# Kernel tuning notes

Hardware: AMD Instinct MI355X
Metric: run time of the kernel (lower is better)

The kernel has to match this reference:

```python
import jax, jax.numpy as jnp
import numpy as np

TOP_K = 2          # n_activated_experts
ROUTE_SCALE = 1.0  # args.route_scale


def setup_inputs() -> dict:
    key = jax.random.key(0)
    ks = jax.random.split(key, 12)
    B, S, D, I, E = 8, 2048, 512, 1024, 8
    SH = 2 * I  # n_shared_experts * moe_inter_dim
    std = 0.02
    return {
        "x": jax.random.normal(ks[0], (B, S, D), jnp.float32),
        "gate_w": (jax.random.normal(ks[1], (E, D), jnp.float32) * std),
        "w1": (jax.random.normal(ks[2], (E, D, I), jnp.float32) * std),
        "w2": (jax.random.normal(ks[3], (E, I, D), jnp.float32) * std),
        "w3": (jax.random.normal(ks[4], (E, D, I), jnp.float32) * std),
        "sw1": (jax.random.normal(ks[5], (D, SH), jnp.float32) * std),
        "sb1": jnp.zeros((SH,), jnp.float32),
        "sw2": (jax.random.normal(ks[6], (SH, D), jnp.float32) * std),
        "sb2": jnp.zeros((D,), jnp.float32),
        "sw3": (jax.random.normal(ks[7], (D, SH), jnp.float32) * std),
        "sb3": jnp.zeros((SH,), jnp.float32),
    }


def reference(x, gate_w, w1, w2, w3, sw1, sb1, sw2, sb2, sw3, sb3):
    B, S, D = x.shape
    xt = x.reshape(-1, D)              # [T, D] tokens
    T = xt.shape[0]
    E = gate_w.shape[0]

    # --- Gate: sigmoid scores, top-k, renormalized weights ---
    scores = jax.nn.sigmoid(xt @ gate_w.T)                 # [T, E]
    topv, topi = jax.lax.top_k(scores, TOP_K)              # [T, K]
    wts = topv / jnp.sum(topv, axis=-1, keepdims=True)
    wts = wts * ROUTE_SCALE

    # Dense combine weights: zero for non-selected experts -> faithful to
    # the torch masked scatter-accumulate over the expert loop.
    cw = jnp.zeros((T, E), xt.dtype).at[jnp.arange(T)[:, None], topi].add(wts)

    # --- Routed SwiGLU experts (ffn_bias=False) ---
    y = jnp.zeros_like(xt)
    for e in range(E):  # fixed small structural loop over experts
        h = jax.nn.silu(xt @ w1[e]) * (xt @ w3[e])         # [T, I]
        y = y + cw[:, e:e + 1] * (h @ w2[e])               # combine

    # --- Load-balance aux loss L_ExpBal ---
    counts = jnp.zeros((E,), xt.dtype).at[topi.reshape(-1)].add(1.0)
    f_i = E * counts / (TOP_K * T)
    P_i = cw.sum(axis=0) / T   # per-expert sum of routed weights
    L_ExpBal = jnp.sum(f_i * P_i)

    # --- Shared experts MLP (biased Linear, SwiGLU) ---
    z = (jax.nn.silu(xt @ sw1 + sb1) * (xt @ sw3 + sb3)) @ sw2 + sb2

    return (y + z).reshape(B, S, D), L_ExpBal
```

## Files before the change

kernel.cpp:

```cpp
#include <hip/hip_runtime.h>
#include <math.h>
#include <stdint.h>

#define T_TOK 16384
#define DDIM  512
#define IDIM  1024
#define NEXP  8
#define SHDIM 2048
#define MPAD  34816
#define GBLK  256

typedef unsigned short u16;
typedef short bf16x8 __attribute__((ext_vector_type(8)));
typedef float f32x4 __attribute__((ext_vector_type(4)));

__device__ __forceinline__ u16 f2bf(float f) {
    unsigned u = __float_as_uint(f);
    u += 0x7FFF + ((u >> 16) & 1);
    return (u16)(u >> 16);
}
__device__ __forceinline__ float bf2f(u16 h) {
    return __uint_as_float((unsigned)h << 16);
}

__device__ __forceinline__ void gload_lds16(const void* g, void* l) {
    __builtin_amdgcn_global_load_lds(
        (const __attribute__((address_space(1))) void*)g,
        (__attribute__((address_space(3))) void*)l, 16, 0, 0);
}

__device__ __forceinline__ int ksw(int r) { return (r & 3) ^ ((r >> 2) & 3); }

__global__ void k_zero(int* cursors) {
    int i = threadIdx.x;
    if (i < NEXP) cursors[i] = 0;
}

__global__ __launch_bounds__(256) void k_gate(
    const float* __restrict__ x, const float* __restrict__ gw,
    int* __restrict__ topi, float* __restrict__ wts,
    int* __restrict__ pcnt, float* __restrict__ pps, u16* __restrict__ xb)
{
    __shared__ int   cnt[NEXP];
    __shared__ float ps[NEXP];
    const int tid = threadIdx.x;
    if (tid < NEXP) { cnt[tid] = 0; ps[tid] = 0.f; }
    __syncthreads();
    const int wid = tid >> 6, lane = tid & 63;

    const float4* gw4 = (const float4*)gw;
    float4 g0[NEXP], g1[NEXP];
#pragma unroll
    for (int e = 0; e < NEXP; e++) {
        g0[e] = gw4[e * 128 + lane];
        g1[e] = gw4[e * 128 + 64 + lane];
    }

    const int t0 = blockIdx.x * 64 + wid * 16;
    for (int u = 0; u < 16; u++) {
        int t = t0 + u;
        const float4* xr4 = (const float4*)(x + (size_t)t * DDIM);
        float4 v0 = xr4[lane];
        float4 v1 = xr4[64 + lane];
        ushort4 o0 = { f2bf(v0.x), f2bf(v0.y), f2bf(v0.z), f2bf(v0.w) };
        ushort4 o1 = { f2bf(v1.x), f2bf(v1.y), f2bf(v1.z), f2bf(v1.w) };
        ushort4* xbo = (ushort4*)(xb + (size_t)t * DDIM);
        xbo[lane] = o0;
        xbo[64 + lane] = o1;
        float acc[NEXP];
#pragma unroll
        for (int e = 0; e < NEXP; e++) {
            acc[e] = v0.x * g0[e].x + v0.y * g0[e].y + v0.z * g0[e].z + v0.w * g0[e].w
                   + v1.x * g1[e].x + v1.y * g1[e].y + v1.z * g1[e].z + v1.w * g1[e].w;
        }
#pragma unroll
        for (int e = 0; e < NEXP; e++) {
#pragma unroll
            for (int off = 32; off; off >>= 1) acc[e] += __shfl_xor(acc[e], off, 64);
        }
        if (lane == 0) {
            float s[NEXP];
#pragma unroll
            for (int e = 0; e < NEXP; e++) s[e] = 1.f / (1.f + expf(-acc[e]));
            int i1 = 0; float v1s = s[0];
#pragma unroll
            for (int e = 1; e < NEXP; e++) if (s[e] > v1s) { v1s = s[e]; i1 = e; }
            int i2 = -1; float v2s = -1.f;
#pragma unroll
            for (int e = 0; e < NEXP; e++) if (e != i1 && s[e] > v2s) { v2s = s[e]; i2 = e; }
            float inv = 1.f / (v1s + v2s);
            float wa = v1s * inv, wb = v2s * inv;
            topi[2 * t] = i1; topi[2 * t + 1] = i2;
            wts[2 * t] = wa;  wts[2 * t + 1] = wb;
            atomicAdd(&cnt[i1], 1); atomicAdd(&cnt[i2], 1);
            atomicAdd(&ps[i1], wa); atomicAdd(&ps[i2], wb);
        }
    }
    __syncthreads();
    if (tid < NEXP) {
        pcnt[blockIdx.x * NEXP + tid] = cnt[tid];
        pps[blockIdx.x * NEXP + tid]  = ps[tid];
    }
}

__global__ void k_scan(const int* __restrict__ pcnt, const float* __restrict__ pps,
                       int* __restrict__ off_pad, float* __restrict__ out_loss)
{
    __shared__ int   scnt[8][NEXP];
    __shared__ float sps[8][NEXP];
    int tid = threadIdx.x;
    if (tid < 64) {
        int e = tid & 7, part = tid >> 3;
        int c = 0; float p = 0.f;
        for (int b = part * 32; b < part * 32 + 32; b++) {
            c += pcnt[b * NEXP + e];
            p += pps[b * NEXP + e];
        }
        scnt[part][e] = c; sps[part][e] = p;
    }
    __syncthreads();
    if (tid == 0) {
        int off = 0; float L = 0.f;
        for (int e = 0; e < NEXP; e++) {
            int c = 0; float p = 0.f;
            for (int q = 0; q < 8; q++) { c += scnt[q][e]; p += sps[q][e]; }
            off_pad[e] = off;
            off += (c + 255) & ~255;
            float f = (float)NEXP * (float)c / (float)(2 * T_TOK);
            L += f * (p / (float)T_TOK);
        }
        off_pad[NEXP] = off;
        out_loss[0] = L;
    }
}

__global__ void k_fillperm(int* __restrict__ perm, u16* __restrict__ zpad) {
    int i = blockIdx.x * blockDim.x + threadIdx.x;
    if (i < MPAD) perm[i] = -1;
    if (blockIdx.x == 0 && threadIdx.x < 256) ((unsigned*)zpad)[threadIdx.x] = 0u;
}

__global__ __launch_bounds__(256) void k_scatter(
    const int* __restrict__ topi, const float* __restrict__ wts,
    const int* __restrict__ off_pad, int* __restrict__ cursors,
    int* __restrict__ perm, float* __restrict__ pw, int* __restrict__ inv)
{
    __shared__ int lcnt[NEXP];
    __shared__ int lbase[NEXP];
    int tid = threadIdx.x;
    if (tid < NEXP) lcnt[tid] = 0;
    __syncthreads();
    int t = blockIdx.x * 256 + tid;
    int e0 = topi[2 * t], e1 = topi[2 * t + 1];
    int p0 = atomicAdd(&lcnt[e0], 1);
    int p1 = atomicAdd(&lcnt[e1], 1);
    __syncthreads();
    if (tid < NEXP) lbase[tid] = atomicAdd(&cursors[tid], lcnt[tid]);
    __syncthreads();
    int s0 = off_pad[e0] + lbase[e0] + p0;
    int s1 = off_pad[e1] + lbase[e1] + p1;
    perm[s0] = t; pw[s0] = wts[2 * t];
    perm[s1] = t; pw[s1] = wts[2 * t + 1];
    inv[2 * t] = s0; inv[2 * t + 1] = s1;
}

__global__ __launch_bounds__(256) void k_transpose(const float* __restrict__ src,
                                                   u16* __restrict__ dst, int R, int C,
                                                   int rmul, int radd, int zrows)
{
    __shared__ u16 t[64][68];
    const float* s = src + (size_t)blockIdx.z * R * C;
    u16* d = dst + (size_t)blockIdx.z * zrows * R;
    int r0 = blockIdx.y * 64, c0 = blockIdx.x * 64;
    int tid = threadIdx.x;
    int lr = tid >> 4, lc = (tid & 15) * 4;
#pragma unroll
    for (int u = 0; u < 4; u++) {
        int r = lr + u * 16;
        float4 v = *(const float4*)&s[(size_t)(r0 + r) * C + c0 + lc];
        t[lc + 0][r] = f2bf(v.x);
        t[lc + 1][r] = f2bf(v.y);
        t[lc + 2][r] = f2bf(v.z);
        t[lc + 3][r] = f2bf(v.w);
    }
    __syncthreads();
    int wr = tid >> 4, wc = (tid & 15) * 4;
#pragma unroll
    for (int u = 0; u < 4; u++) {
        int c = wr + u * 16;
        int gc = c0 + c;
        int rp = (gc >> 6) * rmul + (gc & 63) + radd;
        ushort4 o = { t[c][wc], t[c][wc + 1], t[c][wc + 2], t[c][wc + 3] };
        *(ushort4*)&d[(size_t)rp * R + r0 + wc] = o;
    }
}

template<int MODE>
__device__ __forceinline__ void blockmap(int id, int& mt, int& nt) {
    if (MODE == 0) {
        int xcd = id >> 8, p = id & 255;
        int sm = p >> 7, r = p & 127;
        mt = xcd * 8 + sm * 4 + (r & 3);
        nt = r >> 2;
    } else if (MODE == 1) {
        int xcd = id / 272, p = id % 272;
        mt = xcd * 17 + p / 16;
        nt = p % 16;
    } else if (MODE == 2) {
        int xcd = id >> 5, p = id & 31;
        mt = xcd * 8 + (p >> 2);
        nt = p & 3;
    } else {
        int xcd = id / 68, p = id % 68;
        mt = xcd * 17 + (p >> 2);
        nt = p & 3;
    }
}

template<int MODE, bool ROUTED, bool BIAS>
__global__ __launch_bounds__(256, 2) void k_s1(
    const u16* __restrict__ Axb, const u16* __restrict__ Bt,
    const float* __restrict__ bias1, const float* __restrict__ bias3,
    u16* __restrict__ H, int ldh, const int* __restrict__ off_pad,
    const int* __restrict__ perm, const u16* __restrict__ zpad)
{
    __shared__ __align__(16) unsigned char smem[3 * 24576];
    int mt, nt;
    blockmap<MODE>(blockIdx.y * gridDim.x + blockIdx.x, mt, nt);
    const int m0 = mt * 256;
    if (ROUTED && m0 >= off_pad[NEXP]) return;
    const u16* B = Bt;
    if (ROUTED) {
        int e = 0;
        while (off_pad[e + 1] <= m0) e++;
        B += (size_t)e * (2 * IDIM) * DDIM;
    }
    const int n0r = nt * 128;

    const int tid = threadIdx.x;
    const int wm = tid >> 6, lane = tid & 63;
    const int fr = lane & 15, hi = lane >> 4;

    const u16* asrc[4]; const u16* bsrc[2];
    const int grow = tid >> 2;
    const int gsl  = tid & 3;
#pragma unroll
    for (int s = 0; s < 4; s++) {
        int r = s * 64 + grow;
        int goff = (gsl ^ ksw(r)) * 8;
        if (ROUTED) {
            int tok = perm[m0 + r];
            asrc[s] = (tok >= 0 ? Axb + (size_t)tok * DDIM : zpad) + goff;
        } else {
            asrc[s] = Axb + (size_t)(m0 + r) * DDIM + goff;
        }
    }
#pragma unroll
    for (int s = 0; s < 2; s++) {
        int r = s * 64 + grow;
        int goff = (gsl ^ ksw(r)) * 8;
        bsrc[s] = B + (size_t)(n0r + r) * DDIM + goff;
    }
    const int dstT = tid * 16;

    int aoff[4], boff[8];
#pragma unroll
    for (int i = 0; i < 4; i++) {
        int ar = wm * 64 + i * 16 + fr;
        aoff[i] = ar * 64 + ((hi ^ ksw(ar)) << 4);
    }
#pragma unroll
    for (int j = 0; j < 8; j++) {
        int br = j * 16 + fr;
        boff[j] = 16384 + br * 64 + ((hi ^ ksw(br)) << 4);
    }

    f32x4 acc[4][8];
#pragma unroll
    for (int i = 0; i < 4; i++)
#pragma unroll
        for (int j = 0; j < 8; j++) acc[i][j] = {0.f, 0.f, 0.f, 0.f};

    const int NT = DDIM / 32;
#pragma unroll
    for (int t = 0; t < 2; t++) {
        unsigned char* bb = smem + t * 24576;
#pragma unroll
        for (int s = 0; s < 4; s++) gload_lds16(asrc[s] + t * 32, bb + s * 4096 + dstT);
#pragma unroll
        for (int s = 0; s < 2; s++) gload_lds16(bsrc[s] + t * 32, bb + 16384 + s * 4096 + dstT);
    }

    int bufc = 0;
    for (int t = 0; t < NT; t++) {
        int bufn = bufc + 2; if (bufn >= 3) bufn -= 3;
        if (t + 2 < NT) {
            unsigned char* bb = smem + bufn * 24576;
            int k2 = (t + 2) * 32;
#pragma unroll
            for (int s = 0; s < 4; s++) gload_lds16(asrc[s] + k2, bb + s * 4096 + dstT);
#pragma unroll
            for (int s = 0; s < 2; s++) gload_lds16(bsrc[s] + k2, bb + 16384 + s * 4096 + dstT);
            asm volatile("s_waitcnt vmcnt(12)" ::: "memory");
        } else if (t + 2 == NT) {
            asm volatile("s_waitcnt vmcnt(6)" ::: "memory");
        } else {
            asm volatile("s_waitcnt vmcnt(0)" ::: "memory");
        }
        __builtin_amdgcn_s_barrier();
        __builtin_amdgcn_sched_barrier(0);
        const unsigned char* cb = smem + bufc * 24576;
        bf16x8 av[4], bv[8];
#pragma unroll
        for (int i = 0; i < 4; i++) av[i] = *(const bf16x8*)(cb + aoff[i]);
#pragma unroll
        for (int j = 0; j < 8; j++) bv[j] = *(const bf16x8*)(cb + boff[j]);
        __builtin_amdgcn_s_setprio(1);
#pragma unroll
        for (int i = 0; i < 4; i++)
#pragma unroll
            for (int j = 0; j < 8; j++)
                acc[i][j] = __builtin_amdgcn_mfma_f32_16x16x32_bf16(av[i], bv[j], acc[i][j], 0, 0, 0);
        __builtin_amdgcn_s_setprio(0);
        __builtin_amdgcn_sched_barrier(0);
        __builtin_amdgcn_s_barrier();
        bufc++; if (bufc >= 3) bufc -= 3;
    }

#pragma unroll
    for (int i = 0; i < 4; i++) {
#pragma unroll
        for (int j = 0; j < 4; j++) {
            int hcol = nt * 64 + j * 16 + fr;
            float b1 = BIAS ? bias1[hcol] : 0.f;
            float b3 = BIAS ? bias3[hcol] : 0.f;
#pragma unroll
            for (int r = 0; r < 4; r++) {
                int row = m0 + wm * 64 + i * 16 + hi * 4 + r;
                float v1 = acc[i][j][r] + b1;
                float v3 = acc[i][j + 4][r] + b3;
                float hv = (v1 / (1.f + __expf(-v1))) * v3;
                H[(size_t)row * ldh + hcol] = f2bf(hv);
            }
        }
    }
}

template<int K, int MODE, bool ROUTED>
__global__ __launch_bounds__(256, 2) void k_s2(
    const u16* __restrict__ A, const u16* __restrict__ Bt,
    const float* __restrict__ bias2, float* __restrict__ out,
    u16* __restrict__ ytmp, const int* __restrict__ off_pad)
{
    __shared__ __align__(16) unsigned char smem[3 * 24576];
    int mt, nt;
    blockmap<MODE>(blockIdx.y * gridDim.x + blockIdx.x, mt, nt);
    const int m0 = mt * 256;
    const int n0 = nt * 128;
    if (ROUTED && m0 >= off_pad[NEXP]) return;
    const u16* bt = Bt;
    if (ROUTED) {
        int e = 0;
        while (off_pad[e + 1] <= m0) e++;
        bt += (size_t)e * DDIM * IDIM;
    }
    const int tid = threadIdx.x;
    const int wm = tid >> 6, lane = tid & 63;
    const int fr = lane & 15, hi = lane >> 4;

    const u16* asrc[4]; const u16* bsrc[2];
    const int grow = tid >> 2;
    const int gsl  = tid & 3;
#pragma unroll
    for (int s = 0; s < 4; s++) {
        int r = s * 64 + grow;
        asrc[s] = A + (size_t)(m0 + r) * K + (gsl ^ ksw(r)) * 8;
    }
#pragma unroll
    for (int s = 0; s < 2; s++) {
        int r = s * 64 + grow;
        bsrc[s] = bt + (size_t)(n0 + r) * K + (gsl ^ ksw(r)) * 8;
    }
    const int dstT = tid * 16;

    int aoff[4], boff[8];
#pragma unroll
    for (int i = 0; i < 4; i++) {
        int ar = wm * 64 + i * 16 + fr;
        aoff[i] = ar * 64 + ((hi ^ ksw(ar)) << 4);
    }
#pragma unroll
    for (int j = 0; j < 8; j++) {
        int br = j * 16 + fr;
        boff[j] = 16384 + br * 64 + ((hi ^ ksw(br)) << 4);
    }

    f32x4 acc[4][8];
#pragma unroll
    for (int i = 0; i < 4; i++)
#pragma unroll
        for (int j = 0; j < 8; j++) acc[i][j] = {0.f, 0.f, 0.f, 0.f};

    const int NT = K / 32;
#pragma unroll
    for (int t = 0; t < 2; t++) {
        unsigned char* bb = smem + t * 24576;
#pragma unroll
        for (int s = 0; s < 4; s++) gload_lds16(asrc[s] + t * 32, bb + s * 4096 + dstT);
#pragma unroll
        for (int s = 0; s < 2; s++) gload_lds16(bsrc[s] + t * 32, bb + 16384 + s * 4096 + dstT);
    }

    int bufc = 0;
    for (int t = 0; t < NT; t++) {
        int bufn = bufc + 2; if (bufn >= 3) bufn -= 3;
        if (t + 2 < NT) {
            unsigned char* bb = smem + bufn * 24576;
            int k2 = (t + 2) * 32;
#pragma unroll
            for (int s = 0; s < 4; s++) gload_lds16(asrc[s] + k2, bb + s * 4096 + dstT);
#pragma unroll
            for (int s = 0; s < 2; s++) gload_lds16(bsrc[s] + k2, bb + 16384 + s * 4096 + dstT);
            asm volatile("s_waitcnt vmcnt(12)" ::: "memory");
        } else if (t + 2 == NT) {
            asm volatile("s_waitcnt vmcnt(6)" ::: "memory");
        } else {
            asm volatile("s_waitcnt vmcnt(0)" ::: "memory");
        }
        __builtin_amdgcn_s_barrier();
        __builtin_amdgcn_sched_barrier(0);
        const unsigned char* cb = smem + bufc * 24576;
        bf16x8 av[4], bv[8];
#pragma unroll
        for (int i = 0; i < 4; i++) av[i] = *(const bf16x8*)(cb + aoff[i]);
#pragma unroll
        for (int j = 0; j < 8; j++) bv[j] = *(const bf16x8*)(cb + boff[j]);
        __builtin_amdgcn_s_setprio(1);
#pragma unroll
        for (int i = 0; i < 4; i++)
#pragma unroll
            for (int j = 0; j < 8; j++)
                acc[i][j] = __builtin_amdgcn_mfma_f32_16x16x32_bf16(av[i], bv[j], acc[i][j], 0, 0, 0);
        __builtin_amdgcn_s_setprio(0);
        __builtin_amdgcn_sched_barrier(0);
        __builtin_amdgcn_s_barrier();
        bufc++; if (bufc >= 3) bufc -= 3;
    }

#pragma unroll
    for (int i = 0; i < 4; i++) {
#pragma unroll
        for (int r = 0; r < 4; r++) {
            int row = m0 + wm * 64 + i * 16 + hi * 4 + r;
#pragma unroll
            for (int j = 0; j < 8; j++) {
                int col = n0 + j * 16 + fr;
                float v = acc[i][j][r];
                if (ROUTED) {
                    ytmp[(size_t)row * DDIM + col] = f2bf(v);
                } else {
                    out[(size_t)row * DDIM + col] = v + bias2[col];
                }
            }
        }
    }
}

__global__ __launch_bounds__(256) void k_combine(
    const u16* __restrict__ ytmp, const int* __restrict__ inv,
    const float* __restrict__ wts, float* __restrict__ out)
{
    int idx = blockIdx.x * 256 + threadIdx.x;
    int t = idx >> 7;
    int c = (idx & 127) * 4;
    int s0 = inv[2 * t], s1 = inv[2 * t + 1];
    float w0 = wts[2 * t], w1 = wts[2 * t + 1];
    ushort4 a = *(const ushort4*)&ytmp[(size_t)s0 * DDIM + c];
    ushort4 b = *(const ushort4*)&ytmp[(size_t)s1 * DDIM + c];
    float4 o = *(float4*)&out[(size_t)t * DDIM + c];
    o.x += w0 * bf2f(a.x) + w1 * bf2f(b.x);
    o.y += w0 * bf2f(a.y) + w1 * bf2f(b.y);
    o.z += w0 * bf2f(a.z) + w1 * bf2f(b.z);
    o.w += w0 * bf2f(a.w) + w1 * bf2f(b.w);
    *(float4*)&out[(size_t)t * DDIM + c] = o;
}

extern "C" void kernel_launch(void* const* d_in, const int* in_sizes, int n_in,
                              void* d_out, int out_size, void* d_ws, size_t ws_size,
                              hipStream_t stream)
{
    const float* x   = (const float*)d_in[0];
    const float* gw  = (const float*)d_in[1];
    const float* w1  = (const float*)d_in[2];
    const float* w2  = (const float*)d_in[3];
    const float* w3  = (const float*)d_in[4];
    const float* sw1 = (const float*)d_in[5];
    const float* sb1 = (const float*)d_in[6];
    const float* sw2 = (const float*)d_in[7];
    const float* sb2 = (const float*)d_in[8];
    const float* sw3 = (const float*)d_in[9];
    const float* sb3 = (const float*)d_in[10];
    float* out = (float*)d_out;

    char* ws = (char*)d_ws;
    size_t off = 0;
    int*   topi    = (int*)(ws + off);   off += (size_t)2 * T_TOK * 4;
    float* wts     = (float*)(ws + off); off += (size_t)2 * T_TOK * 4;
    int*   perm    = (int*)(ws + off);   off += (size_t)MPAD * 4;
    float* pw      = (float*)(ws + off); off += (size_t)MPAD * 4;
    int*   cursors = (int*)(ws + off);   off += 256;
    int*   off_pad = (int*)(ws + off);   off += 256;
    int*   pcnt    = (int*)(ws + off);   off += (size_t)GBLK * NEXP * 4;
    float* pps     = (float*)(ws + off); off += (size_t)GBLK * NEXP * 4;
    int*   inv     = (int*)(ws + off);   off += (size_t)2 * T_TOK * 4;
    u16*   zpad    = (u16*)(ws + off);   off += 1024;
    u16*   xb      = (u16*)(ws + off);   off += (size_t)T_TOK * DDIM * 2;
    u16*   ytmp    = (u16*)(ws + off);   off += (size_t)MPAD * DDIM * 2;
    u16*   w13Ts   = (u16*)(ws + off);   off += (size_t)2 * SHDIM * DDIM * 2;
    u16*   w13Tr   = (u16*)(ws + off);   off += (size_t)NEXP * 2 * IDIM * DDIM * 2;
    u16*   w2T     = (u16*)(ws + off);   off += (size_t)NEXP * DDIM * IDIM * 2;
    u16*   sw2T    = (u16*)(ws + off);   off += (size_t)DDIM * SHDIM * 2;
    u16*   hb      = (u16*)(ws + off);   off += (size_t)MPAD * IDIM * 2;

    k_zero<<<1, 64, 0, stream>>>(cursors);
    k_gate<<<GBLK, 256, 0, stream>>>(x, gw, topi, wts, pcnt, pps, xb);
    k_scan<<<1, 64, 0, stream>>>(pcnt, pps, off_pad, out + (size_t)T_TOK * DDIM);
    k_fillperm<<<MPAD / 256, 256, 0, stream>>>(perm, zpad);
    k_scatter<<<T_TOK / 256, 256, 0, stream>>>(topi, wts, off_pad, cursors, perm, pw, inv);

    k_transpose<<<dim3(SHDIM / 64, DDIM / 64, 1), 256, 0, stream>>>(sw1, w13Ts, DDIM, SHDIM, 128, 0,  2 * SHDIM);
    k_transpose<<<dim3(SHDIM / 64, DDIM / 64, 1), 256, 0, stream>>>(sw3, w13Ts, DDIM, SHDIM, 128, 64, 2 * SHDIM);
    k_transpose<<<dim3(IDIM / 64, DDIM / 64, NEXP), 256, 0, stream>>>(w1, w13Tr, DDIM, IDIM, 128, 0,  2 * IDIM);
    k_transpose<<<dim3(IDIM / 64, DDIM / 64, NEXP), 256, 0, stream>>>(w3, w13Tr, DDIM, IDIM, 128, 64, 2 * IDIM);
    k_transpose<<<dim3(DDIM / 64, IDIM / 64, NEXP), 256, 0, stream>>>(w2, w2T, IDIM, DDIM, 64, 0, DDIM);
    k_transpose<<<dim3(DDIM / 64, SHDIM / 64, 1), 256, 0, stream>>>(sw2, sw2T, SHDIM, DDIM, 64, 0, DDIM);

    k_s1<0, false, true><<<dim3(32, 64), 256, 0, stream>>>(
        xb, w13Ts, sb1, sb3, hb, SHDIM, nullptr, nullptr, nullptr);
    k_s2<SHDIM, 2, false><<<dim3(4, 64), 256, 0, stream>>>(
        hb, sw2T, sb2, out, nullptr, nullptr);
    k_s1<1, true, false><<<dim3(16, 136), 256, 0, stream>>>(
        xb, w13Tr, nullptr, nullptr, hb, IDIM, off_pad, perm, zpad);
    k_s2<IDIM, 3, true><<<dim3(4, 136), 256, 0, stream>>>(
        hb, w2T, nullptr, nullptr, ytmp, off_pad);
    k_combine<<<(T_TOK * DDIM / 4) / 256, 256, 0, stream>>>(ytmp, inv, wts, out);
}
```

Before: 376.5 us.

## Unify GEMM kernels into 8-wave k_mm with K=64 tiles and split-phase prefetch

Replaces the separate s1/s2 GEMM kernels with one templated 512-thread kernel that uses a 256x128 tile. Each step now covers K=64 instead of 32, with a new XOR swizzle and interleaved w1/w3 columns at 16-column granularity. The per-step work is split into two half-M phases, and the global-to-LDS prefetch is spread across them. Block mapping switches to a generic XCD round-robin swizzle. The aim is fewer barriers per K, better latency hiding and simpler code, at the cost of 144KB of LDS per block, which may limit occupancy to one block per CU.

```diff
diff --git a/kernel.cpp b/kernel.cpp
--- a/kernel.cpp
+++ b/kernel.cpp
@@ -8,6 +8,7 @@
 #define NEXP  8
 #define SHDIM 2048
 #define MPAD  34816
+#define NMT_R 136
 #define GBLK  256
 
 typedef unsigned short u16;
@@ -29,7 +30,11 @@
         (__attribute__((address_space(3))) void*)l, 16, 0, 0);
 }
 
-__device__ __forceinline__ int ksw(int r) { return (r & 3) ^ ((r >> 2) & 3); }
+__device__ __forceinline__ int xcd_swz(int id, int nwg) {
+    return (id & 7) * (nwg >> 3) + (id >> 3);
+}
+
+__device__ __forceinline__ int fsw(int r) { return (r >> 1) & 7; }
 
 __global__ void k_zero(int* cursors) {
     int i = threadIdx.x;
@@ -166,7 +171,7 @@
 
 __global__ __launch_bounds__(256) void k_transpose(const float* __restrict__ src,
                                                    u16* __restrict__ dst, int R, int C,
-                                                   int rmul, int radd, int zrows)
+                                                   int lg, int rmul, int radd, int zrows)
 {
     __shared__ u16 t[64][68];
     const float* s = src + (size_t)blockIdx.z * R * C;
@@ -189,277 +194,191 @@
     for (int u = 0; u < 4; u++) {
         int c = wr + u * 16;
         int gc = c0 + c;
-        int rp = (gc >> 6) * rmul + (gc & 63) + radd;
+        int rp = (gc >> lg) * rmul + (gc & ((1 << lg) - 1)) + radd;
         ushort4 o = { t[c][wc], t[c][wc + 1], t[c][wc + 2], t[c][wc + 3] };
         *(ushort4*)&d[(size_t)rp * R + r0 + wc] = o;
     }
 }
 
-template<int MODE>
-__device__ __forceinline__ void blockmap(int id, int& mt, int& nt) {
-    if (MODE == 0) {
-        int xcd = id >> 8, p = id & 255;
-        int sm = p >> 7, r = p & 127;
-        mt = xcd * 8 + sm * 4 + (r & 3);
-        nt = r >> 2;
-    } else if (MODE == 1) {
-        int xcd = id / 272, p = id % 272;
-        mt = xcd * 17 + p / 16;
-        nt = p % 16;
-    } else if (MODE == 2) {
-        int xcd = id >> 5, p = id & 31;
-        mt = xcd * 8 + (p >> 2);
-        nt = p & 3;
-    } else {
-        int xcd = id / 68, p = id % 68;
-        mt = xcd * 17 + (p >> 2);
-        nt = p & 3;
-    }
-}
-
-template<int MODE, bool ROUTED, bool BIAS>
-__global__ __launch_bounds__(256, 2) void k_s1(
-    const u16* __restrict__ Axb, const u16* __restrict__ Bt,
+template<int K, int EPI, bool ROUTED, bool BIAS>
+__global__ __launch_bounds__(512, 2) void k_mm(
+    const u16* __restrict__ A, const u16* __restrict__ Bt,
     const float* __restrict__ bias1, const float* __restrict__ bias3,
-    u16* __restrict__ H, int ldh, const int* __restrict__ off_pad,
-    const int* __restrict__ perm, const u16* __restrict__ zpad)
-{
-    __shared__ __align__(16) unsigned char smem[3 * 24576];
-    int mt, nt;
-    blockmap<MODE>(blockIdx.y * gridDim.x + blockIdx.x, mt, nt);
-    const int m0 = mt * 256;
+    u16* __restrict__ H, int ldh, float* __restrict__ outp,
+    const int* __restrict__ off_pad, const int* __restrict__ perm,
+    const u16* __restrict__ zpad, int bstride)
+{
+    __shared__ __align__(16) unsigned char smem[3 * 49152];
+    const int nwg = gridDim.x * gridDim.y;
+    const int id  = xcd_swz(blockIdx.y * gridDim.x + blockIdx.x, nwg);
+    const int m0  = (id / gridDim.x) * 256;
+    const int ntb = id % gridDim.x;
+    const int n0r = ntb * 128;
     if (ROUTED && m0 >= off_pad[NEXP]) return;
     const u16* B = Bt;
     if (ROUTED) {
         int e = 0;
         while (off_pad[e + 1] <= m0) e++;
-        B += (size_t)e * (2 * IDIM) * DDIM;
-    }
-    const int n0r = nt * 128;
-
+        B += (size_t)e * bstride;
+    }
     const int tid = threadIdx.x;
-    const int wm = tid >> 6, lane = tid & 63;
+    const int wid = tid >> 6, lane = tid & 63;
+    const int wm = wid >> 2, wn = wid & 3;
     const int fr = lane & 15, hi = lane >> 4;
 
     const u16* asrc[4]; const u16* bsrc[2];
-    const int grow = tid >> 2;
-    const int gsl  = tid & 3;
+    const int srow = tid >> 3, sslot = tid & 7;
 #pragma unroll
     for (int s = 0; s < 4; s++) {
-        int r = s * 64 + grow;
-        int goff = (gsl ^ ksw(r)) * 8;
-        if (ROUTED) {
+        int r = s * 64 + srow;
+        int goff = (sslot ^ fsw(r)) * 8;
+        if (EPI == 0 && ROUTED) {
             int tok = perm[m0 + r];
-            asrc[s] = (tok >= 0 ? Axb + (size_t)tok * DDIM : zpad) + goff;
+            asrc[s] = (tok >= 0 ? A + (size_t)tok * K : zpad) + goff;
         } else {
-            asrc[s] = Axb + (size_t)(m0 + r) * DDIM + goff;
+            asrc[s] = A + (size_t)(m0 + r) * K + goff;
         }
     }
 #pragma unroll
     for (int s = 0; s < 2; s++) {
-        int r = s * 64 + grow;
-        int goff = (gsl ^ ksw(r)) * 8;
-        bsrc[s] = B + (size_t)(n0r + r) * DDIM + goff;
+        int r = s * 64 + srow;
+        bsrc[s] = B + (size_t)(n0r + r) * K + (sslot ^ fsw(r)) * 8;
     }
     const int dstT = tid * 16;
 
-    int aoff[4], boff[8];
-#pragma unroll
-    for (int i = 0; i < 4; i++) {
-        int ar = wm * 64 + i * 16 + fr;
-        aoff[i] = ar * 64 + ((hi ^ ksw(ar)) << 4);
-    }
-#pragma unroll
-    for (int j = 0; j < 8; j++) {
-        int br = j * 16 + fr;
-        boff[j] = 16384 + br * 64 + ((hi ^ ksw(br)) << 4);
-    }
-
-    f32x4 acc[4][8];
-#pragma unroll
-    for (int i = 0; i < 4; i++)
-#pragma unroll
-        for (int j = 0; j < 8; j++) acc[i][j] = {0.f, 0.f, 0.f, 0.f};
-
-    const int NT = DDIM / 32;
+    int aoff[2][4][2], boff[2][2];
+#pragma unroll
+    for (int h = 0; h < 2; h++)
+#pragma unroll
+        for (int i = 0; i < 4; i++) {
+            int ar = wm * 128 + h * 64 + i * 16 + fr;
+#pragma unroll
+            for (int s = 0; s < 2; s++)
+                aoff[h][i][s] = ar * 128 + (((s * 4 + hi) ^ fsw(ar)) << 4);
+        }
+#pragma unroll
+    for (int j = 0; j < 2; j++) {
+        int br = wn * 32 + j * 16 + fr;
+#pragma unroll
+        for (int s = 0; s < 2; s++)
+            boff[j][s] = 32768 + br * 128 + (((s * 4 + hi) ^ fsw(br)) << 4);
+    }
+
+    f32x4 acc[8][2];
+#pragma unroll
+    for (int i = 0; i < 8; i++)
+#pragma unroll
+        for (int j = 0; j < 2; j++) acc[i][j] = {0.f, 0.f, 0.f, 0.f};
+
+    const int NT = K / 64;
 #pragma unroll
     for (int t = 0; t < 2; t++) {
-        unsigned char* bb = smem + t * 24576;
-#pragma unroll
-        for (int s = 0; s < 4; s++) gload_lds16(asrc[s] + t * 32, bb + s * 4096 + dstT);
-#pragma unroll
-        for (int s = 0; s < 2; s++) gload_lds16(bsrc[s] + t * 32, bb + 16384 + s * 4096 + dstT);
-    }
+        unsigned char* bb = smem + t * 49152;
+#pragma unroll
+        for (int s = 0; s < 4; s++) gload_lds16(asrc[s] + t * 64, bb + s * 8192 + dstT);
+#pragma unroll
+        for (int s = 0; s < 2; s++) gload_lds16(bsrc[s] + t * 64, bb + 32768 + s * 8192 + dstT);
+    }
+    asm volatile("s_waitcnt vmcnt(6)" ::: "memory");
+    __builtin_amdgcn_s_barrier();
 
     int bufc = 0;
     for (int t = 0; t < NT; t++) {
+        const unsigned char* cb = smem + bufc * 49152;
         int bufn = bufc + 2; if (bufn >= 3) bufn -= 3;
-        if (t + 2 < NT) {
-            unsigned char* bb = smem + bufn * 24576;
-            int k2 = (t + 2) * 32;
-#pragma unroll
-            for (int s = 0; s < 4; s++) gload_lds16(asrc[s] + k2, bb + s * 4096 + dstT);
-#pragma unroll
-            for (int s = 0; s < 2; s++) gload_lds16(bsrc[s] + k2, bb + 16384 + s * 4096 + dstT);
-            asm volatile("s_waitcnt vmcnt(12)" ::: "memory");
-        } else if (t + 2 == NT) {
-            asm volatile("s_waitcnt vmcnt(6)" ::: "memory");
-        } else {
-            asm volatile("s_waitcnt vmcnt(0)" ::: "memory");
-        }
-        __builtin_amdgcn_s_barrier();
-        __builtin_amdgcn_sched_barrier(0);
-        const unsigned char* cb = smem + bufc * 24576;
-        bf16x8 av[4], bv[8];
-#pragma unroll
-        for (int i = 0; i < 4; i++) av[i] = *(const bf16x8*)(cb + aoff[i]);
-#pragma unroll
-        for (int j = 0; j < 8; j++) bv[j] = *(const bf16x8*)(cb + boff[j]);
-        __builtin_amdgcn_s_setprio(1);
-#pragma unroll
-        for (int i = 0; i < 4; i++)
-#pragma unroll
-            for (int j = 0; j < 8; j++)
-                acc[i][j] = __builtin_amdgcn_mfma_f32_16x16x32_bf16(av[i], bv[j], acc[i][j], 0, 0, 0);
-        __builtin_amdgcn_s_setprio(0);
-        __builtin_amdgcn_sched_barrier(0);
-        __builtin_amdgcn_s_barrier();
+        unsigned char* nb = smem + bufn * 49152;
+        const int k2 = (t + 2) * 64;
+        bf16x8 bv[2][2];
+
+        {
+            bf16x8 av[4][2];
+#pragma unroll
+            for (int j = 0; j < 2; j++)
+#pragma unroll
+                for (int s = 0; s < 2; s++) bv[j][s] = *(const bf16x8*)(cb + boff[j][s]);
+#pragma unroll
+            for (int i = 0; i < 4; i++)
+#pragma unroll
+                for (int s = 0; s < 2; s++) av[i][s] = *(const bf16x8*)(cb + aoff[0][i][s]);
+            if (t + 2 < NT) {
+#pragma unroll
+                for (int s = 0; s < 3; s++) gload_lds16(asrc[s] + k2, nb + s * 8192 + dstT);
+            }
+            __builtin_amdgcn_s_barrier();
+            asm volatile("s_waitcnt lgkmcnt(0)" ::: "memory");
+            __builtin_amdgcn_sched_barrier(0);
+            __builtin_amdgcn_s_setprio(1);
+#pragma unroll
+            for (int s = 0; s < 2; s++)
+#pragma unroll
+                for (int i = 0; i < 4; i++)
+#pragma unroll
+                    for (int j = 0; j < 2; j++)
+                        acc[i][j] = __builtin_amdgcn_mfma_f32_16x16x32_bf16(av[i][s], bv[j][s], acc[i][j], 0, 0, 0);
+            __builtin_amdgcn_s_setprio(0);
+            __builtin_amdgcn_sched_barrier(0);
+            __builtin_amdgcn_s_barrier();
+        }
+
+        {
+            bf16x8 av[4][2];
+#pragma unroll
+            for (int i = 0; i < 4; i++)
+#pragma unroll
+                for (int s = 0; s < 2; s++) av[i][s] = *(const bf16x8*)(cb + aoff[1][i][s]);
+            if (t + 2 < NT) {
+                gload_lds16(asrc[3] + k2, nb + 3 * 8192 + dstT);
+#pragma unroll
+                for (int s = 0; s < 2; s++) gload_lds16(bsrc[s] + k2, nb + 32768 + s * 8192 + dstT);
+                asm volatile("s_waitcnt vmcnt(6)" ::: "memory");
+            } else if (t + 2 == NT) {
+                asm volatile("s_waitcnt vmcnt(0)" ::: "memory");
+            }
+            __builtin_amdgcn_s_barrier();
+            asm volatile("s_waitcnt lgkmcnt(0)" ::: "memory");
+            __builtin_amdgcn_sched_barrier(0);
+            __builtin_amdgcn_s_setprio(1);
+#pragma unroll
+            for (int s = 0; s < 2; s++)
+#pragma unroll
+                for (int i = 0; i < 4; i++)
+#pragma unroll
+                    for (int j = 0; j < 2; j++)
+                        acc[4 + i][j] = __builtin_amdgcn_mfma_f32_16x16x32_bf16(av[i][s], bv[j][s], acc[4 + i][j], 0, 0, 0);
+            __builtin_amdgcn_s_setprio(0);
+            __builtin_amdgcn_sched_barrier(0);
+            __builtin_amdgcn_s_barrier();
+        }
         bufc++; if (bufc >= 3) bufc -= 3;
     }
 
-#pragma unroll
-    for (int i = 0; i < 4; i++) {
-#pragma unroll
-        for (int j = 0; j < 4; j++) {
-            int hcol = nt * 64 + j * 16 + fr;
-            float b1 = BIAS ? bias1[hcol] : 0.f;
-            float b3 = BIAS ? bias3[hcol] : 0.f;
+    if (EPI == 0) {
+        int hcol = ntb * 64 + wn * 16 + fr;
+        float b1 = BIAS ? bias1[hcol] : 0.f;
+        float b3 = BIAS ? bias3[hcol] : 0.f;
+#pragma unroll
+        for (int i = 0; i < 8; i++) {
 #pragma unroll
             for (int r = 0; r < 4; r++) {
-                int row = m0 + wm * 64 + i * 16 + hi * 4 + r;
-                float v1 = acc[i][j][r] + b1;
-                float v3 = acc[i][j + 4][r] + b3;
+                int row = m0 + wm * 128 + i * 16 + hi * 4 + r;
+                float v1 = acc[i][0][r] + b1;
+                float v3 = acc[i][1][r] + b3;
                 float hv = (v1 / (1.f + __expf(-v1))) * v3;
                 H[(size_t)row * ldh + hcol] = f2bf(hv);
             }
         }
-    }
-}
-
-template<int K, int MODE, bool ROUTED>
-__global__ __launch_bounds__(256, 2) void k_s2(
-    const u16* __restrict__ A, const u16* __restrict__ Bt,
-    const float* __restrict__ bias2, float* __restrict__ out,
-    u16* __restrict__ ytmp, const int* __restrict__ off_pad)
-{
-    __shared__ __align__(16) unsigned char smem[3 * 24576];
-    int mt, nt;
-    blockmap<MODE>(blockIdx.y * gridDim.x + blockIdx.x, mt, nt);
-    const int m0 = mt * 256;
-    const int n0 = nt * 128;
-    if (ROUTED && m0 >= off_pad[NEXP]) return;
-    const u16* bt = Bt;
-    if (ROUTED) {
-        int e = 0;
-        while (off_pad[e + 1] <= m0) e++;
-        bt += (size_t)e * DDIM * IDIM;
-    }
-    const int tid = threadIdx.x;
-    const int wm = tid >> 6, lane = tid & 63;
-    const int fr = lane & 15, hi = lane >> 4;
-
-    const u16* asrc[4]; const u16* bsrc[2];
-    const int grow = tid >> 2;
-    const int gsl  = tid & 3;
-#pragma unroll
-    for (int s = 0; s < 4; s++) {
-        int r = s * 64 + grow;
-        asrc[s] = A + (size_t)(m0 + r) * K + (gsl ^ ksw(r)) * 8;
-    }
-#pragma unroll
-    for (int s = 0; s < 2; s++) {
-        int r = s * 64 + grow;
-        bsrc[s] = bt + (size_t)(n0 + r) * K + (gsl ^ ksw(r)) * 8;
-    }
-    const int dstT = tid * 16;
-
-    int aoff[4], boff[8];
-#pragma unroll
-    for (int i = 0; i < 4; i++) {
-        int ar = wm * 64 + i * 16 + fr;
-        aoff[i] = ar * 64 + ((hi ^ ksw(ar)) << 4);
-    }
-#pragma unroll
-    for (int j = 0; j < 8; j++) {
-        int br = j * 16 + fr;
-        boff[j] = 16384 + br * 64 + ((hi ^ ksw(br)) << 4);
-    }
-
-    f32x4 acc[4][8];
-#pragma unroll
-    for (int i = 0; i < 4; i++)
-#pragma unroll
-        for (int j = 0; j < 8; j++) acc[i][j] = {0.f, 0.f, 0.f, 0.f};
-
-    const int NT = K / 32;
-#pragma unroll
-    for (int t = 0; t < 2; t++) {
-        unsigned char* bb = smem + t * 24576;
-#pragma unroll
-        for (int s = 0; s < 4; s++) gload_lds16(asrc[s] + t * 32, bb + s * 4096 + dstT);
-#pragma unroll
-        for (int s = 0; s < 2; s++) gload_lds16(bsrc[s] + t * 32, bb + 16384 + s * 4096 + dstT);
-    }
-
-    int bufc = 0;
-    for (int t = 0; t < NT; t++) {
-        int bufn = bufc + 2; if (bufn >= 3) bufn -= 3;
-        if (t + 2 < NT) {
-            unsigned char* bb = smem + bufn * 24576;
-            int k2 = (t + 2) * 32;
-#pragma unroll
-            for (int s = 0; s < 4; s++) gload_lds16(asrc[s] + k2, bb + s * 4096 + dstT);
-#pragma unroll
-            for (int s = 0; s < 2; s++) gload_lds16(bsrc[s] + k2, bb + 16384 + s * 4096 + dstT);
-            asm volatile("s_waitcnt vmcnt(12)" ::: "memory");
-        } else if (t + 2 == NT) {
-            asm volatile("s_waitcnt vmcnt(6)" ::: "memory");
-        } else {
-            asm volatile("s_waitcnt vmcnt(0)" ::: "memory");
-        }
-        __builtin_amdgcn_s_barrier();
-        __builtin_amdgcn_sched_barrier(0);
-        const unsigned char* cb = smem + bufc * 24576;
-        bf16x8 av[4], bv[8];
-#pragma unroll
-        for (int i = 0; i < 4; i++) av[i] = *(const bf16x8*)(cb + aoff[i]);
-#pragma unroll
-        for (int j = 0; j < 8; j++) bv[j] = *(const bf16x8*)(cb + boff[j]);
-        __builtin_amdgcn_s_setprio(1);
-#pragma unroll
-        for (int i = 0; i < 4; i++)
-#pragma unroll
-            for (int j = 0; j < 8; j++)
-                acc[i][j] = __builtin_amdgcn_mfma_f32_16x16x32_bf16(av[i], bv[j], acc[i][j], 0, 0, 0);
-        __builtin_amdgcn_s_setprio(0);
-        __builtin_amdgcn_sched_barrier(0);
-        __builtin_amdgcn_s_barrier();
-        bufc++; if (bufc >= 3) bufc -= 3;
-    }
-
-#pragma unroll
-    for (int i = 0; i < 4; i++) {
-#pragma unroll
-        for (int r = 0; r < 4; r++) {
-            int row = m0 + wm * 64 + i * 16 + hi * 4 + r;
-#pragma unroll
-            for (int j = 0; j < 8; j++) {
-                int col = n0 + j * 16 + fr;
-                float v = acc[i][j][r];
-                if (ROUTED) {
-                    ytmp[(size_t)row * DDIM + col] = f2bf(v);
-                } else {
-                    out[(size_t)row * DDIM + col] = v + bias2[col];
+    } else {
+#pragma unroll
+        for (int i = 0; i < 8; i++) {
+#pragma unroll
+            for (int r = 0; r < 4; r++) {
+                int row = m0 + wm * 128 + i * 16 + hi * 4 + r;
+#pragma unroll
+                for (int j = 0; j < 2; j++) {
+                    int col = n0r + wn * 32 + j * 16 + fr;
+                    float v = acc[i][j][r];
+                    if (EPI == 1) outp[(size_t)row * DDIM + col] = v + bias1[col];
+                    else          H[(size_t)row * DDIM + col] = f2bf(v);
                 }
             }
         }
@@ -528,20 +447,20 @@
     k_fillperm<<<MPAD / 256, 256, 0, stream>>>(perm, zpad);
     k_scatter<<<T_TOK / 256, 256, 0, stream>>>(topi, wts, off_pad, cursors, perm, pw, inv);
 
-    k_transpose<<<dim3(SHDIM / 64, DDIM / 64, 1), 256, 0, stream>>>(sw1, w13Ts, DDIM, SHDIM, 128, 0,  2 * SHDIM);
-    k_transpose<<<dim3(SHDIM / 64, DDIM / 64, 1), 256, 0, stream>>>(sw3, w13Ts, DDIM, SHDIM, 128, 64, 2 * SHDIM);
-    k_transpose<<<dim3(IDIM / 64, DDIM / 64, NEXP), 256, 0, stream>>>(w1, w13Tr, DDIM, IDIM, 128, 0,  2 * IDIM);
-    k_transpose<<<dim3(IDIM / 64, DDIM / 64, NEXP), 256, 0, stream>>>(w3, w13Tr, DDIM, IDIM, 128, 64, 2 * IDIM);
-    k_transpose<<<dim3(DDIM / 64, IDIM / 64, NEXP), 256, 0, stream>>>(w2, w2T, IDIM, DDIM, 64, 0, DDIM);
-    k_transpose<<<dim3(DDIM / 64, SHDIM / 64, 1), 256, 0, stream>>>(sw2, sw2T, SHDIM, DDIM, 64, 0, DDIM);
-
-    k_s1<0, false, true><<<dim3(32, 64), 256, 0, stream>>>(
-        xb, w13Ts, sb1, sb3, hb, SHDIM, nullptr, nullptr, nullptr);
-    k_s2<SHDIM, 2, false><<<dim3(4, 64), 256, 0, stream>>>(
-        hb, sw2T, sb2, out, nullptr, nullptr);
-    k_s1<1, true, false><<<dim3(16, 136), 256, 0, stream>>>(
-        xb, w13Tr, nullptr, nullptr, hb, IDIM, off_pad, perm, zpad);
-    k_s2<IDIM, 3, true><<<dim3(4, 136), 256, 0, stream>>>(
-        hb, w2T, nullptr, nullptr, ytmp, off_pad);
+    k_transpose<<<dim3(SHDIM / 64, DDIM / 64, 1), 256, 0, stream>>>(sw1, w13Ts, DDIM, SHDIM, 4, 32, 0,  2 * SHDIM);
+    k_transpose<<<dim3(SHDIM / 64, DDIM / 64, 1), 256, 0, stream>>>(sw3, w13Ts, DDIM, SHDIM, 4, 32, 16, 2 * SHDIM);
+    k_transpose<<<dim3(IDIM / 64, DDIM / 64, NEXP), 256, 0, stream>>>(w1, w13Tr, DDIM, IDIM, 4, 32, 0,  2 * IDIM);
+    k_transpose<<<dim3(IDIM / 64, DDIM / 64, NEXP), 256, 0, stream>>>(w3, w13Tr, DDIM, IDIM, 4, 32, 16, 2 * IDIM);
+    k_transpose<<<dim3(DDIM / 64, IDIM / 64, NEXP), 256, 0, stream>>>(w2, w2T, IDIM, DDIM, 6, 64, 0, DDIM);
+    k_transpose<<<dim3(DDIM / 64, SHDIM / 64, 1), 256, 0, stream>>>(sw2, sw2T, SHDIM, DDIM, 6, 64, 0, DDIM);
+
+    k_mm<DDIM, 0, false, true><<<dim3(SHDIM / 64, T_TOK / 256), 512, 0, stream>>>(
+        xb, w13Ts, sb1, sb3, hb, SHDIM, nullptr, nullptr, nullptr, nullptr, 0);
+    k_mm<SHDIM, 1, false, false><<<dim3(DDIM / 128, T_TOK / 256), 512, 0, stream>>>(
+        hb, sw2T, sb2, nullptr, nullptr, 0, out, nullptr, nullptr, nullptr, 0);
+    k_mm<DDIM, 0, true, false><<<dim3(IDIM / 64, NMT_R), 512, 0, stream>>>(
+        xb, w13Tr, nullptr, nullptr, hb, IDIM, nullptr, off_pad, perm, zpad, 2 * IDIM * DDIM);
+    k_mm<IDIM, 2, true, false><<<dim3(DDIM / 128, NMT_R), 512, 0, stream>>>(
+        hb, w2T, nullptr, nullptr, ytmp, 0, nullptr, off_pad, nullptr, nullptr, DDIM * IDIM);
     k_combine<<<(T_TOK * DDIM / 4) / 256, 256, 0, stream>>>(ytmp, inv, wts, out);
 }
```

Measured after the change: 368.5 us. 2.1% less time.
